# Kernel optimization log

Measured on AMD Instinct MI355X. Metric: run time of the kernel, lower is better.

## Reference

```python
import jax, jax.numpy as jnp
import numpy as np

LATENT_DIM = 128
HIDDEN = 20
BATCH = 32768


def _lstm_cell(x, h, c, W_ih, W_hh, b_ih, b_hh):
    # torch.nn.LSTMCell: gates order (i, f, g, o)
    gates = x @ W_ih.T + b_ih + h @ W_hh.T + b_hh
    i, f, g, o = jnp.split(gates, 4, axis=1)
    c_new = jax.nn.sigmoid(f) * c + jax.nn.sigmoid(i) * jnp.tanh(g)
    h_new = jax.nn.sigmoid(o) * jnp.tanh(c_new)
    return h_new, c_new


def setup_inputs() -> dict:
    key = jax.random.key(0)
    ks = jax.random.split(key, 10)
    L, H = LATENT_DIM, HIDDEN

    def u(k, shape, fan):  # torch LSTMCell init: U(-1/sqrt(hidden), 1/sqrt(hidden))
        b = 1.0 / np.sqrt(fan)
        return jax.random.uniform(k, shape, jnp.float32, -b, b)

    return {
        "mu": jax.random.normal(ks[0], (BATCH, L), jnp.float32),
        "log_var": jax.random.normal(ks[1], (BATCH, L), jnp.float32),
        "W_ih1": u(ks[2], (4 * H, L - 1), H),
        "W_hh1": u(ks[3], (4 * H, H), H),
        "b_ih1": u(ks[4], (4 * H,), H),
        "b_hh1": u(ks[5], (4 * H,), H),
        "W_ih2": u(ks[6], (8, 2 * H), 2),
        "W_hh2": u(ks[7], (8, 2), 2),
        "b_ih2": u(ks[8], (8,), 2),
        "b_hh2": u(ks[9], (8,), 2),
    }


def reference(mu, log_var, W_ih1, W_hh1, b_ih1, b_hh1, W_ih2, W_hh2, b_ih2, b_hh2):
    # sample=False path (the module's default)
    B, L = mu.shape
    H = W_hh1.shape[1]
    dt = mu.dtype
    # fixed reparameterization noise: eps[0] for the first draw, eps[k] for step k
    eps = jax.random.normal(jax.random.key(42), (L, B), dt)

    first_input = eps[0] * jnp.exp(0.5 * log_var[:, 0]) + mu[:, 0]  # [B]
    inp0 = jnp.zeros((B, L - 1), dt).at[:, 0].set(first_input)
    cols = jnp.arange(L - 1)
    mu_trunc = mu[:, : L - 1]

    def step(carry, xs):
        h1, c1, h2, c2, inp = carry
        idx, eps_t = xs
        h1, c1 = _lstm_cell(inp, h1, c1, W_ih1, W_hh1, b_ih1, b_hh1)
        out1 = jax.nn.leaky_relu(jnp.concatenate([h1, c1], axis=1))  # slope 0.01
        h2, c2 = _lstm_cell(out1, h2, c2, W_ih2, W_hh2, b_ih2, b_hh2)
        mu_r, lv_r = h2[:, 0], h2[:, 1]
        samp = eps_t * jnp.exp(0.5 * lv_r) + mu_r
        # next input = mu[:, :idx+1] zero-padded to width L-1 (sample=False branch)
        new_inp = jnp.where(cols <= idx, mu_trunc, jnp.zeros((), dt))
        return (h1, c1, h2, c2, new_inp), (mu_r, lv_r, samp)

    z = lambda n: jnp.zeros((B, n), dt)
    carry0 = (z(H), z(H), z(2), z(2), inp0)
    _, (mus, lvs, smps) = jax.lax.scan(step, carry0, (jnp.arange(1, L), eps[1:]))

    mus_full = jnp.concatenate([jnp.zeros((B, 1), dt), mus.T], axis=1)   # [B, L]
    lvs_full = jnp.concatenate([jnp.ones((B, 1), dt), lvs.T], axis=1)    # [B, L]
    samples = jnp.concatenate([first_input[:, None], smps.T], axis=1)    # [B, L]
    return mus_full, lvs_full, samples
```

## Files before the change

kernel.cpp:

```cpp
#include <hip/hip_runtime.h>
#include <stdint.h>
#include <math.h>

#define BATCH 32768
#define LDIM 128
#define HID 20

#define WS_AW  0
#define WS_AU  1280
#define WS_WCD 1792
#define WS_TOTAL 11952


__device__ __forceinline__ void threefry2x32(uint32_t x0, uint32_t x1,
                                             uint32_t& o0, uint32_t& o1) {
  const uint32_t k0 = 0u, k1 = 42u;
  const uint32_t k2 = k0 ^ k1 ^ 0x1BD11BDAu;
  uint32_t v0 = x0 + k0, v1 = x1 + k1;
#define TF_R(r) { v0 += v1; v1 = (v1 << (r)) | (v1 >> (32 - (r))); v1 ^= v0; }
  TF_R(13) TF_R(15) TF_R(26) TF_R(6)
  v0 += k1; v1 += k2 + 1u;
  TF_R(17) TF_R(29) TF_R(16) TF_R(24)
  v0 += k2; v1 += k0 + 2u;
  TF_R(13) TF_R(15) TF_R(26) TF_R(6)
  v0 += k0; v1 += k1 + 3u;
  TF_R(17) TF_R(29) TF_R(16) TF_R(24)
  v0 += k1; v1 += k2 + 4u;
  TF_R(13) TF_R(15) TF_R(26) TF_R(6)
  v0 += k2; v1 += k0 + 5u;
#undef TF_R
  o0 = v0; o1 = v1;
}

__device__ __forceinline__ float erfinv_xla_f32(float x) {
  float t = __fmul_rn(x, x);
  float w = -(float)log1p(-(double)t);
  float p;
  if (w < 5.0f) {
    w = __fadd_rn(w, -2.5f);
    p = 2.81022636e-08f;
    p = __fadd_rn(__fmul_rn(p, w), 3.43273939e-07f);
    p = __fadd_rn(__fmul_rn(p, w), -3.5233877e-06f);
    p = __fadd_rn(__fmul_rn(p, w), -4.39150654e-06f);
    p = __fadd_rn(__fmul_rn(p, w), 0.00021858087f);
    p = __fadd_rn(__fmul_rn(p, w), -0.00125372503f);
    p = __fadd_rn(__fmul_rn(p, w), -0.00417768164f);
    p = __fadd_rn(__fmul_rn(p, w), 0.246640727f);
    p = __fadd_rn(__fmul_rn(p, w), 1.50140941f);
  } else {
    w = __fadd_rn(__fsqrt_rn(w), -3.0f);
    p = -0.000200214257f;
    p = __fadd_rn(__fmul_rn(p, w), 0.000100950558f);
    p = __fadd_rn(__fmul_rn(p, w), 0.00134934322f);
    p = __fadd_rn(__fmul_rn(p, w), -0.00367342844f);
    p = __fadd_rn(__fmul_rn(p, w), 0.00573950773f);
    p = __fadd_rn(__fmul_rn(p, w), -0.0076224613f);
    p = __fadd_rn(__fmul_rn(p, w), 0.00943887047f);
    p = __fadd_rn(__fmul_rn(p, w), 1.00167406f);
    p = __fadd_rn(__fmul_rn(p, w), 2.83297682f);
  }
  return __fmul_rn(p, x);
}

__device__ __forceinline__ float eps_val(int t, int b) {
  uint32_t n = (uint32_t)t * 32768u + (uint32_t)b;
  uint32_t o0, o1;
  threefry2x32(0u, n, o0, o1);
  uint32_t bits = o0 ^ o1;
  const float lo    = __uint_as_float(0xBF7FFFFFu);
  const float sqrt2 = __uint_as_float(0x3FB504F3u);
  float f = __fadd_rn(__uint_as_float((bits >> 9) | 0x3F800000u), -1.0f);
  float u = __fadd_rn(__fmul_rn(f, 2.0f), lo);
  u = fmaxf(u, lo);
  return __fmul_rn(sqrt2, erfinv_xla_f32(u));
}

__device__ __forceinline__ float fexp2(float x) { return __builtin_amdgcn_exp2f(x); }
__device__ __forceinline__ float frcp(float x)  { return __builtin_amdgcn_rcpf(x); }
__device__ __forceinline__ float fexp(float x)  { return fexp2(1.442695040888963f * x); }
__device__ __forceinline__ float sigm(float x)  { return frcp(1.0f + fexp2(-1.442695040888963f * x)); }
__device__ __forceinline__ float tanhx(float x) { return 1.0f - 2.0f * frcp(1.0f + fexp2(2.885390081777926f * x)); }

typedef _Float16 f16x8 __attribute__((ext_vector_type(8)));
typedef _Float16 f16x2 __attribute__((ext_vector_type(2)));
typedef float    f32x4 __attribute__((ext_vector_type(4)));

__device__ __forceinline__ uint32_t packh(float x, float y) {
  f16x2 p;
  p.x = (_Float16)x;
  p.y = (_Float16)y;
  return __builtin_bit_cast(uint32_t, p);
}

__global__ void repack_kernel(const float* __restrict__ W_ih1,
                              const float* __restrict__ W_hh1,
                              const float* __restrict__ W_ih2,
                              float* __restrict__ ws) {
  uint32_t* wsu = (uint32_t*)ws;
  const int stride = gridDim.x * blockDim.x;
  const int tid0 = blockIdx.x * blockDim.x + threadIdx.x;
  for (int idx = tid0; idx < 1280; idx += stride) {
    int q = idx & 3, l = (idx >> 2) & 63, m = idx >> 8;
    int rA = l & 15, koct = l >> 4;
    int ty = rA & 3, u = 4 * m + (rA >> 2);
    int k0 = koct * 8 + 2 * q, k1 = k0 + 1;
    float w0 = (k0 < 20) ? W_hh1[(ty * 20 + u) * 20 + k0] : 0.0f;
    float w1 = (k1 < 20) ? W_hh1[(ty * 20 + u) * 20 + k1] : 0.0f;
    wsu[WS_AW + idx] = packh(w0, w1);
  }
  for (int idx = tid0; idx < 512; idx += stride) {
    int q = idx & 3, l = (idx >> 2) & 63, ks = idx >> 8;
    int j = l & 15, koct = l >> 4;
    int kk0 = ks * 32 + koct * 8 + 2 * q, kk1 = kk0 + 1;
    float w0 = (j < 8 && kk0 < 40)
                   ? W_ih2[j * 40 + (kk0 & 1) * 20 + (kk0 >> 1)] : 0.0f;
    float w1 = (j < 8 && kk1 < 40)
                   ? W_ih2[j * 40 + (kk1 & 1) * 20 + (kk1 >> 1)] : 0.0f;
    wsu[WS_AU + idx] = packh(w0, w1);
  }
  for (int idx = tid0; idx < 10160; idx += stride) {
    int grow = idx % 80, col = idx / 80;
    int u = grow >> 2, ty = grow & 3;
    ws[WS_WCD + idx] = W_ih1[(ty * 20 + u) * 127 + col];
  }
}

__global__ __launch_bounds__(256, 1) void sampler_kernel(
    const float* __restrict__ mu, const float* __restrict__ log_var,
    const float* __restrict__ ws,
    const float* __restrict__ b_ih1, const float* __restrict__ b_hh1,
    const float* __restrict__ W_hh2,
    const float* __restrict__ b_ih2, const float* __restrict__ b_hh2,
    float* __restrict__ out) {
  __shared__ float WcL[10160];
  __shared__ __align__(16) _Float16 hsh[4][640];
  __shared__ __align__(16) _Float16 lsh[4][1152];

  const int tid  = threadIdx.x;
  const int lane = tid & 63;
  const int wvl  = __builtin_amdgcn_readfirstlane(tid >> 6);
  const int sub  = lane >> 4;
  const int el   = lane & 15;
  const int elem = blockIdx.x * 64 + wvl * 16 + el;

  for (int i = tid; i < 10160; i += 256) WcL[i] = ws[WS_WCD + i];
  {
    uint32_t* hz = (uint32_t*)&hsh[0][0];
    for (int i = tid; i < 1280; i += 256) hz[i] = 0u;
    uint32_t* lz = (uint32_t*)&lsh[0][0];
    for (int i = tid; i < 2304; i += 256) lz[i] = 0u;
  }

  const uint32_t* wsu = (const uint32_t*)ws;
  f16x8 aw[5], au[2];
#pragma unroll
  for (int m = 0; m < 5; ++m)
    aw[m] = *(const f16x8*)(wsu + WS_AW + (m * 64 + lane) * 4);
#pragma unroll
  for (int ks = 0; ks < 2; ++ks)
    au[ks] = *(const f16x8*)(wsu + WS_AU + (ks * 64 + lane) * 4);

  __syncthreads();

  _Float16* hrow = &hsh[wvl][el * 40];
  _Float16* lrow = &lsh[wvl][el * 72];

  const float* mrow = mu + (size_t)elem * LDIM;

  float w2[16], b2s[8];
#pragma unroll
  for (int i = 0; i < 16; ++i) w2[i] = W_hh2[i];
#pragma unroll
  for (int i = 0; i < 8; ++i)  b2s[i] = b_ih2[i] + b_hh2[i];

  float eps0 = eps_val(0, elem);
  float m0 = mrow[0];
  float fi = fmaf(eps0, fexp(0.5f * log_var[(size_t)elem * LDIM]), m0);

  f32x4 acc[5];
#pragma unroll
  for (int m = 0; m < 5; ++m) {
    f32x4 w0 = *(const f32x4*)&WcL[16 * m + 4 * sub];
#pragma unroll
    for (int r = 0; r < 4; ++r) {
      const int grow = 16 * m + 4 * sub + r;
      const int g = (grow & 3) * 20 + (grow >> 2);
      acc[m][r] = fmaf(fi, w0[r], b_ih1[g] + b_hh1[g]);
    }
  }

  float cst[5];
#pragma unroll
  for (int m = 0; m < 5; ++m) cst[m] = 0.0f;
  float h2a = 0.0f, h2b = 0.0f, c2a = 0.0f, c2b = 0.0f;

  float* out_mu = out;
  float* out_lv = out + (size_t)BATCH * LDIM;
  float* out_sp = out + 2 * (size_t)BATCH * LDIM;
  const size_t rowoff = (size_t)elem * LDIM;
  if (sub == 0)      { out_mu[rowoff] = 0.0f; out_lv[rowoff] = 1.0f; }
  else if (sub == 1) { out_sp[rowoff] = fi; }

  const f32x4 z4 = {0.0f, 0.0f, 0.0f, 0.0f};
  float xm_pref = m0;
  float eps4 = 0.0f;

  for (int t = 1; t < LDIM; ++t) {
    float xm = xm_pref;
    xm_pref = mrow[t];

    if (((t - 1) & 3) == 0) eps4 = eps_val(t + sub, elem);

    if (t >= 2) {
      if (t == 2) {
        float d0 = m0 - fi;
#pragma unroll
        for (int m = 0; m < 5; ++m) {
          f32x4 w0 = *(const f32x4*)&WcL[16 * m + 4 * sub];
#pragma unroll
          for (int r = 0; r < 4; ++r) acc[m][r] = fmaf(d0, w0[r], acc[m][r]);
        }
      }
#pragma unroll
      for (int m = 0; m < 5; ++m) {
        f32x4 wc = *(const f32x4*)&WcL[(t - 1) * 80 + 16 * m + 4 * sub];
#pragma unroll
        for (int r = 0; r < 4; ++r) acc[m][r] = fmaf(xm, wc[r], acc[m][r]);
      }
    }

    f16x8 bh = *(const f16x8*)&hrow[sub * 8];
    f32x4 d[5];
#pragma unroll
    for (int m = 0; m < 5; ++m)
      d[m] = __builtin_amdgcn_mfma_f32_16x16x32_f16(aw[m], bh, acc[m], 0, 0, 0);

#pragma unroll
    for (int m = 0; m < 5; ++m) {
      float ik = sigm(d[m][0]), fk = sigm(d[m][1]);
      float gk = tanhx(d[m][2]), ok = sigm(d[m][3]);
      float cn = fmaf(fk, cst[m], ik * gk);
      cst[m] = cn;
      float hk = ok * tanhx(cn);
      hrow[4 * m + sub] = (_Float16)hk;
      float lh = (hk >= 0.0f) ? hk : 0.01f * hk;
      float lc = (cn >= 0.0f) ? cn : 0.01f * cn;
      f16x2 p; p.x = (_Float16)lh; p.y = (_Float16)lc;
      ((f16x2*)lrow)[4 * m + sub] = p;
    }

    f16x8 bl0 = *(const f16x8*)&lrow[sub * 8];
    f16x8 bl1 = *(const f16x8*)&lrow[32 + sub * 8];
    f32x4 d2 = __builtin_amdgcn_mfma_f32_16x16x32_f16(au[0], bl0, z4, 0, 0, 0);
    d2 = __builtin_amdgcn_mfma_f32_16x16x32_f16(au[1], bl1, d2, 0, 0, 0);
    float e0 = __shfl_xor(d2[0], 16, 64);
    float e1 = __shfl_xor(d2[1], 16, 64);
    float e2 = __shfl_xor(d2[2], 16, 64);
    float e3 = __shfl_xor(d2[3], 16, 64);
    const bool s1 = (sub == 1);
    float v0 = s1 ? e0 : d2[0], v1 = s1 ? e1 : d2[1];
    float v2 = s1 ? e2 : d2[2], v3 = s1 ? e3 : d2[3];
    float v4 = s1 ? d2[0] : e0, v5 = s1 ? d2[1] : e1;
    float v6 = s1 ? d2[2] : e2, v7 = s1 ? d2[3] : e3;

    float g0 = fmaf(h2a, w2[0],  fmaf(h2b, w2[1],  b2s[0])) + v0;
    float g1 = fmaf(h2a, w2[2],  fmaf(h2b, w2[3],  b2s[1])) + v1;
    float g2 = fmaf(h2a, w2[4],  fmaf(h2b, w2[5],  b2s[2])) + v2;
    float g3 = fmaf(h2a, w2[6],  fmaf(h2b, w2[7],  b2s[3])) + v3;
    float g4 = fmaf(h2a, w2[8],  fmaf(h2b, w2[9],  b2s[4])) + v4;
    float g5 = fmaf(h2a, w2[10], fmaf(h2b, w2[11], b2s[5])) + v5;
    float g6 = fmaf(h2a, w2[12], fmaf(h2b, w2[13], b2s[6])) + v6;
    float g7 = fmaf(h2a, w2[14], fmaf(h2b, w2[15], b2s[7])) + v7;

    float i20 = sigm(g0), i21 = sigm(g1);
    float f20 = sigm(g2), f21 = sigm(g3);
    float t20 = tanhx(g4), t21 = tanhx(g5);
    float o20 = sigm(g6), o21 = sigm(g7);
    c2a = fmaf(f20, c2a, i20 * t20);
    c2b = fmaf(f21, c2b, i21 * t21);
    h2a = o20 * tanhx(c2a);
    h2b = o21 * tanhx(c2b);

    float eps_t = __shfl(eps4, ((t - 1) & 3) * 16 + el, 64);
    if (sub == 0) {
      out_mu[rowoff + t] = h2a;
      out_lv[rowoff + t] = h2b;
    } else if (sub == 1) {
      out_sp[rowoff + t] = fmaf(eps_t, fexp(0.5f * h2b), h2a);
    }
  }
}

extern "C" void kernel_launch(void* const* d_in, const int* in_sizes, int n_in,
                              void* d_out, int out_size, void* d_ws, size_t ws_size,
                              hipStream_t stream) {
  (void)in_sizes; (void)n_in; (void)ws_size; (void)out_size;
  const float* mu      = (const float*)d_in[0];
  const float* log_var = (const float*)d_in[1];
  const float* W_ih1   = (const float*)d_in[2];
  const float* W_hh1   = (const float*)d_in[3];
  const float* b_ih1   = (const float*)d_in[4];
  const float* b_hh1   = (const float*)d_in[5];
  const float* W_ih2   = (const float*)d_in[6];
  const float* W_hh2   = (const float*)d_in[7];
  const float* b_ih2   = (const float*)d_in[8];
  const float* b_hh2   = (const float*)d_in[9];
  float* out = (float*)d_out;
  float* ws  = (float*)d_ws;

  repack_kernel<<<dim3(8), dim3(256), 0, stream>>>(W_ih1, W_hh1, W_ih2, ws);
  dim3 grid(BATCH / 64), block(256);
  sampler_kernel<<<grid, block, 0, stream>>>(mu, log_var, ws, b_ih1, b_hh1,
                                             W_hh2, b_ih2, b_hh2, out);
}
```

Baseline: 335.5 us.

## Software-pipeline second LSTM cell one step behind the first

Delays the second LSTM cell's computation for step t-1 into iteration t, so it runs alongside the first cell's MFMA for step t rather than serially after it. The second cell's inputs are read from shared memory before the first cell overwrites them. The eps value for the delayed step is kept in an extra register across the 4-step refresh. The last step is finished after the loop with an explicit eps computation. This aims to break the serial dependency chain inside each iteration and give the scheduler independent work to interleave, at the cost of more live registers.

```diff
diff --git a/kernel.cpp b/kernel.cpp
--- a/kernel.cpp
+++ b/kernel.cpp
@@ -152,13 +152,12 @@
   }
 
   const uint32_t* wsu = (const uint32_t*)ws;
-  f16x8 aw[5], au[2];
+  f16x8 aw[5], au0, au1;
 #pragma unroll
   for (int m = 0; m < 5; ++m)
     aw[m] = *(const f16x8*)(wsu + WS_AW + (m * 64 + lane) * 4);
-#pragma unroll
-  for (int ks = 0; ks < 2; ++ks)
-    au[ks] = *(const f16x8*)(wsu + WS_AU + (ks * 64 + lane) * 4);
+  au0 = *(const f16x8*)(wsu + WS_AU + lane * 4);
+  au1 = *(const f16x8*)(wsu + WS_AU + (64 + lane) * 4);
 
   __syncthreads();
 
@@ -203,13 +202,59 @@
 
   const f32x4 z4 = {0.0f, 0.0f, 0.0f, 0.0f};
   float xm_pref = m0;
-  float eps4 = 0.0f;
+  float eps4 = 0.0f, eps_old = 0.0f;
+
+  auto lstm2_finish = [&](f16x8 bl0, f16x8 bl1, float eps_t, int e) {
+    f32x4 d2 = __builtin_amdgcn_mfma_f32_16x16x32_f16(au0, bl0, z4, 0, 0, 0);
+    d2 = __builtin_amdgcn_mfma_f32_16x16x32_f16(au1, bl1, d2, 0, 0, 0);
+    float e0 = __shfl_xor(d2[0], 16, 64);
+    float e1 = __shfl_xor(d2[1], 16, 64);
+    float e2 = __shfl_xor(d2[2], 16, 64);
+    float e3 = __shfl_xor(d2[3], 16, 64);
+    const bool s1 = (sub == 1);
+    float v0 = s1 ? e0 : d2[0], v1 = s1 ? e1 : d2[1];
+    float v2 = s1 ? e2 : d2[2], v3 = s1 ? e3 : d2[3];
+    float v4 = s1 ? d2[0] : e0, v5 = s1 ? d2[1] : e1;
+    float v6 = s1 ? d2[2] : e2, v7 = s1 ? d2[3] : e3;
+
+    float g0 = fmaf(h2a, w2[0],  fmaf(h2b, w2[1],  b2s[0])) + v0;
+    float g1 = fmaf(h2a, w2[2],  fmaf(h2b, w2[3],  b2s[1])) + v1;
+    float g2 = fmaf(h2a, w2[4],  fmaf(h2b, w2[5],  b2s[2])) + v2;
+    float g3 = fmaf(h2a, w2[6],  fmaf(h2b, w2[7],  b2s[3])) + v3;
+    float g4 = fmaf(h2a, w2[8],  fmaf(h2b, w2[9],  b2s[4])) + v4;
+    float g5 = fmaf(h2a, w2[10], fmaf(h2b, w2[11], b2s[5])) + v5;
+    float g6 = fmaf(h2a, w2[12], fmaf(h2b, w2[13], b2s[6])) + v6;
+    float g7 = fmaf(h2a, w2[14], fmaf(h2b, w2[15], b2s[7])) + v7;
+
+    float i20 = sigm(g0), i21 = sigm(g1);
+    float f20 = sigm(g2), f21 = sigm(g3);
+    float t20 = tanhx(g4), t21 = tanhx(g5);
+    float o20 = sigm(g6), o21 = sigm(g7);
+    c2a = fmaf(f20, c2a, i20 * t20);
+    c2b = fmaf(f21, c2b, i21 * t21);
+    h2a = o20 * tanhx(c2a);
+    h2b = o21 * tanhx(c2b);
+
+    if (sub == 0) {
+      out_mu[rowoff + e] = h2a;
+      out_lv[rowoff + e] = h2b;
+    } else if (sub == 1) {
+      out_sp[rowoff + e] = fmaf(eps_t, fexp(0.5f * h2b), h2a);
+    }
+  };
 
   for (int t = 1; t < LDIM; ++t) {
     float xm = xm_pref;
     xm_pref = mrow[t];
 
-    if (((t - 1) & 3) == 0) eps4 = eps_val(t + sub, elem);
+    const bool refresh = ((t - 1) & 3) == 0;
+    if (refresh) { eps_old = eps4; eps4 = eps_val(t + sub, elem); }
+
+    f16x8 bl0, bl1;
+    if (t >= 2) {
+      bl0 = *(const f16x8*)&lrow[sub * 8];
+      bl1 = *(const f16x8*)&lrow[32 + sub * 8];
+    }
 
     if (t >= 2) {
       if (t == 2) {
@@ -227,6 +272,12 @@
 #pragma unroll
         for (int r = 0; r < 4; ++r) acc[m][r] = fmaf(xm, wc[r], acc[m][r]);
       }
+    }
+
+    if (t >= 2) {
+      float src = refresh ? eps_old : eps4;
+      float eps_t = __shfl(src, ((t - 2) & 3) * 16 + el, 64);
+      lstm2_finish(bl0, bl1, eps_t, t - 1);
     }
 
     f16x8 bh = *(const f16x8*)&hrow[sub * 8];
@@ -248,46 +299,13 @@
       f16x2 p; p.x = (_Float16)lh; p.y = (_Float16)lc;
       ((f16x2*)lrow)[4 * m + sub] = p;
     }
-
+  }
+
+  {
     f16x8 bl0 = *(const f16x8*)&lrow[sub * 8];
     f16x8 bl1 = *(const f16x8*)&lrow[32 + sub * 8];
-    f32x4 d2 = __builtin_amdgcn_mfma_f32_16x16x32_f16(au[0], bl0, z4, 0, 0, 0);
-    d2 = __builtin_amdgcn_mfma_f32_16x16x32_f16(au[1], bl1, d2, 0, 0, 0);
-    float e0 = __shfl_xor(d2[0], 16, 64);
-    float e1 = __shfl_xor(d2[1], 16, 64);
-    float e2 = __shfl_xor(d2[2], 16, 64);
-    float e3 = __shfl_xor(d2[3], 16, 64);
-    const bool s1 = (sub == 1);
-    float v0 = s1 ? e0 : d2[0], v1 = s1 ? e1 : d2[1];
-    float v2 = s1 ? e2 : d2[2], v3 = s1 ? e3 : d2[3];
-    float v4 = s1 ? d2[0] : e0, v5 = s1 ? d2[1] : e1;
-    float v6 = s1 ? d2[2] : e2, v7 = s1 ? d2[3] : e3;
-
-    float g0 = fmaf(h2a, w2[0],  fmaf(h2b, w2[1],  b2s[0])) + v0;
-    float g1 = fmaf(h2a, w2[2],  fmaf(h2b, w2[3],  b2s[1])) + v1;
-    float g2 = fmaf(h2a, w2[4],  fmaf(h2b, w2[5],  b2s[2])) + v2;
-    float g3 = fmaf(h2a, w2[6],  fmaf(h2b, w2[7],  b2s[3])) + v3;
-    float g4 = fmaf(h2a, w2[8],  fmaf(h2b, w2[9],  b2s[4])) + v4;
-    float g5 = fmaf(h2a, w2[10], fmaf(h2b, w2[11], b2s[5])) + v5;
-    float g6 = fmaf(h2a, w2[12], fmaf(h2b, w2[13], b2s[6])) + v6;
-    float g7 = fmaf(h2a, w2[14], fmaf(h2b, w2[15], b2s[7])) + v7;
-
-    float i20 = sigm(g0), i21 = sigm(g1);
-    float f20 = sigm(g2), f21 = sigm(g3);
-    float t20 = tanhx(g4), t21 = tanhx(g5);
-    float o20 = sigm(g6), o21 = sigm(g7);
-    c2a = fmaf(f20, c2a, i20 * t20);
-    c2b = fmaf(f21, c2b, i21 * t21);
-    h2a = o20 * tanhx(c2a);
-    h2b = o21 * tanhx(c2b);
-
-    float eps_t = __shfl(eps4, ((t - 1) & 3) * 16 + el, 64);
-    if (sub == 0) {
-      out_mu[rowoff + t] = h2a;
-      out_lv[rowoff + t] = h2b;
-    } else if (sub == 1) {
-      out_sp[rowoff + t] = fmaf(eps_t, fexp(0.5f * h2b), h2a);
-    }
+    float eps_t = eps_val(127, elem);
+    lstm2_finish(bl0, bl1, eps_t, 127);
   }
 }
 
```

Result: no change. 336.8 us (+0.4%).
